# Kernel tuning notes

Measured on AMD Instinct MI355X. Metric: run time of the kernel, lower is better.

The kernel has to match this reference:

```python
import jax, jax.numpy as jnp
import numpy as np

DECAY = 0.99
EPS = 1e-5
BETA = 0.25

def _l2norm(v, axis=-1):
    # F.normalize: x / max(||x||, 1e-12)
    n = jnp.sqrt(jnp.sum(v * v, axis=axis, keepdims=True))
    return v / jnp.maximum(n, 1e-12)

def setup_inputs() -> dict:
    key = jax.random.key(0)
    k0, k1, k2, k3 = jax.random.split(key, 4)
    B, C, H, W, E, K = 8, 256, 64, 64, 32, 8192
    x = jax.random.normal(k0, (B, C, H, W), jnp.float32)
    Wq = jax.random.normal(k1, (E, C), jnp.float32) * 0.05  # 1x1 conv kernel
    bq = jnp.zeros((E,), jnp.float32)
    emb = jax.random.normal(k2, (K, E), jnp.float32)
    emb = _l2norm(emb, axis=1)  # matches F.normalize init in __init__
    ema_cluster_size = jnp.ones((K,), jnp.float32)
    ema_weight = emb  # consistent post-init EMA state
    return {"x": x, "Wq": Wq, "bq": bq, "embedding": emb,
            "ema_cluster_size": ema_cluster_size, "ema_weight": ema_weight}

def reference(x, Wq, bq, embedding, ema_cluster_size, ema_weight):
    B, C, H, W = x.shape
    E = Wq.shape[0]
    K = embedding.shape[0]
    # quant_conv: 1x1 conv == per-pixel linear
    z = jnp.einsum('bchw,ec->behw', x, Wq) + bq[None, :, None, None]  # [B,E,H,W]
    z_flat = z.transpose(0, 2, 3, 1).reshape(-1, E)  # [N,E]
    # get_idx(use_znorm=True): cosine similarity argmax (== argmin L2 on normalized)
    zn = _l2norm(z_flat, axis=1)
    en = _l2norm(embedding, axis=1)
    indices = jnp.argmax(zn @ en.T, axis=1)  # [N]
    # codebook gather (raw embedding, as in torch)
    z_q = embedding[indices].reshape(B, H, W, E).transpose(0, 3, 1, 2)  # [B,E,H,W]
    # EMA update (training path; scatter == one-hot.T @ z_flat / one-hot.sum)
    counts = jax.ops.segment_sum(jnp.ones((z_flat.shape[0],), z_flat.dtype), indices, num_segments=K)
    dw = jax.ops.segment_sum(z_flat, indices, num_segments=K)  # [K,E]
    new_cs = DECAY * ema_cluster_size + (1.0 - DECAY) * counts
    new_w = DECAY * ema_weight + (1.0 - DECAY) * dw
    n = jnp.sum(new_cs)
    cs_smoothed = (new_cs + EPS) / (n + K * EPS) * n
    new_embedding = new_w / cs_smoothed[:, None]
    # commitment loss + straight-through
    qloss = BETA * jnp.mean((jax.lax.stop_gradient(z_q) - z) ** 2)
    z_q_st = z + jax.lax.stop_gradient(z_q - z)
    return (z_q_st, indices.reshape(B, H, W), qloss, new_embedding, new_cs, new_w)
```

## Files before the change

### kernel.cpp

```cpp
#include <hip/hip_runtime.h>

#define B_ 8
#define C_ 256
#define HW_ 4096
#define E_ 32
#define K_ 8192
#define N_ 32768
#define NCHUNK 4
#define KC_ (K_ / NCHUNK)
#define NSTAGE (KC_ / 128)
#define KSEG 32
#define PIX 128

#define DECAY_ 0.99f
#define OMD_   0.01f
#define EPS_   1e-5f
#define BETA_  0.25f

#define O_ZQ   0
#define O_IDX  1048576
#define O_QL   1081344
#define O_NEMB 1081345
#define O_NCS  1343489
#define O_NW   1351681

#define WS_EH   0u
#define WS_EM   131072u
#define WS_Z    262144u
#define WS_PACK 1310720u
#define WS_PCS  1572864u
#define WS_QP   1572992u

typedef float f32x4 __attribute__((ext_vector_type(4)));
typedef short s16x8 __attribute__((ext_vector_type(8)));
typedef unsigned long long u64;

__device__ __forceinline__ unsigned short f2bf(float f) {
    unsigned u = __float_as_uint(f);
    u = u + 0x7fffu + ((u >> 16) & 1u);
    return (unsigned short)(u >> 16);
}
__device__ __forceinline__ float bf2f(unsigned short h) {
    return __uint_as_float(((unsigned)h) << 16);
}
__device__ __forceinline__ unsigned ford(float f) {
    unsigned u = __float_as_uint(f);
    return (u & 0x80000000u) ? ~u : (u | 0x80000000u);
}
__device__ __forceinline__ int imax(int a, int b) { return a > b ? a : b; }
__device__ __forceinline__ int imin(int a, int b) { return a < b ? a : b; }

__device__ __forceinline__ void gload_lds16(const void* g, void* l) {
    __builtin_amdgcn_global_load_lds(
        (const __attribute__((address_space(1))) unsigned int*)g,
        (__attribute__((address_space(3))) unsigned int*)l, 16, 0, 0);
}

__global__ __launch_bounds__(256) void k_pre(const float* __restrict__ emb,
                                             const float* __restrict__ cs,
                                             uint4* __restrict__ eh16,
                                             uint4* __restrict__ em16,
                                             float* __restrict__ part_cs,
                                             const float* __restrict__ x,
                                             const float* __restrict__ Wq,
                                             const float* __restrict__ bq,
                                             float* __restrict__ zout) {
    __shared__ float wqt[C_ * E_];
    int tid = threadIdx.x;

    if (blockIdx.x < 128) {
        int t4 = blockIdx.x * 256 + tid;
        int k = t4 >> 2, q = t4 & 3;
        const float4* r = (const float4*)(emb + (size_t)k * E_ + q * 8);
        float4 u0 = r[0], u1 = r[1];
        float ss = u0.x*u0.x + u0.y*u0.y + u0.z*u0.z + u0.w*u0.w
                 + u1.x*u1.x + u1.y*u1.y + u1.z*u1.z + u1.w*u1.w;
        ss += __shfl_xor(ss, 1, 64);
        ss += __shfl_xor(ss, 2, 64);
        float inv = 1.0f / fmaxf(sqrtf(ss), 1e-12f);

        float v[8] = {u0.x, u0.y, u0.z, u0.w, u1.x, u1.y, u1.z, u1.w};
        unsigned short h1a[8], h2a[8];
#pragma unroll
        for (int e = 0; e < 8; e++) {
            float en = v[e] * inv;
            unsigned short h1 = f2bf(en);
            float r1 = en - bf2f(h1);
            h1a[e] = h1; h2a[e] = f2bf(r1);
        }
        int t = k >> 4, c15 = k & 15;
        eh16[t * 64 + q * 16 + c15] = ((uint4*)h1a)[0];
        em16[t * 64 + q * 16 + c15] = ((uint4*)h2a)[0];

        if (tid < 64) {
            float cv = cs[blockIdx.x * 64 + tid];
#pragma unroll
            for (int off = 32; off > 0; off >>= 1) cv += __shfl_down(cv, off);
            if (tid == 0) part_cs[blockIdx.x] = cv;
        }
        return;
    }

    int zb = blockIdx.x - 128;
#pragma unroll
    for (int i = 0; i < 32; i++) {
        int g = i * 256 + tid;
        int e = g >> 8;
        int c = g & 255;
        wqt[c * E_ + e] = Wq[g];
    }
    __syncthreads();
    int lp = tid & 63, eg = tid >> 6;
    int n0 = zb * 128 + lp;
    int b  = n0 >> 12, hw = n0 & (HW_ - 1);
    const float* xp = x + (size_t)b * C_ * HW_ + hw;
    float a[16];
#pragma unroll
    for (int j = 0; j < 16; j++) a[j] = 0.f;
#pragma unroll 4
    for (int c = 0; c < C_; c++) {
        float xa = xp[(size_t)c * HW_];
        float xb = xp[(size_t)c * HW_ + 64];
        const float4* wr = (const float4*)(wqt + c * E_ + eg * 8);
        float4 w0 = wr[0], w1 = wr[1];
        a[0]  += xa * w0.x; a[1]  += xa * w0.y; a[2]  += xa * w0.z; a[3]  += xa * w0.w;
        a[4]  += xa * w1.x; a[5]  += xa * w1.y; a[6]  += xa * w1.z; a[7]  += xa * w1.w;
        a[8]  += xb * w0.x; a[9]  += xb * w0.y; a[10] += xb * w0.z; a[11] += xb * w0.w;
        a[12] += xb * w1.x; a[13] += xb * w1.y; a[14] += xb * w1.z; a[15] += xb * w1.w;
    }
    float bqv[8];
#pragma unroll
    for (int j = 0; j < 8; j++) bqv[j] = bq[eg * 8 + j];
    float4* zgA = (float4*)(zout + (size_t)n0 * E_ + eg * 8);
    float4* zgB = (float4*)(zout + (size_t)(n0 + 64) * E_ + eg * 8);
    zgA[0] = make_float4(a[0]+bqv[0],  a[1]+bqv[1],  a[2]+bqv[2],  a[3]+bqv[3]);
    zgA[1] = make_float4(a[4]+bqv[4],  a[5]+bqv[5],  a[6]+bqv[6],  a[7]+bqv[7]);
    zgB[0] = make_float4(a[8]+bqv[0],  a[9]+bqv[1],  a[10]+bqv[2], a[11]+bqv[3]);
    zgB[1] = make_float4(a[12]+bqv[4], a[13]+bqv[5], a[14]+bqv[6], a[15]+bqv[7]);
}

__global__ __launch_bounds__(512) void k_score_mfma(const float* __restrict__ zws,
                                                    const char* __restrict__ ehb,
                                                    const char* __restrict__ emb_b,
                                                    int2* __restrict__ pk2) {
    __shared__ __align__(16) char smem[32768];

    int tid  = threadIdx.x;
    int lane = tid & 63;
    int w    = tid >> 6;
    int chunk = blockIdx.y;

    s16x8 a1, a2;
    {
        int ploc = w * 16 + (lane & 15);
        int n0   = blockIdx.x * PIX + ploc;
        int e0   = (lane >> 4) * 8;
        const float4* zp = (const float4*)(zws + (size_t)n0 * E_ + e0);
        float4 z0 = zp[0], z1 = zp[1];
        float zz[8] = {z0.x, z0.y, z0.z, z0.w, z1.x, z1.y, z1.z, z1.w};
#pragma unroll
        for (int j = 0; j < 8; j++) {
            float zv = zz[j] * 134217728.0f;
            unsigned short h1 = f2bf(zv);
            float r1 = zv - bf2f(h1);
            a1[j] = (short)h1; a2[j] = (short)f2bf(r1);
        }
    }

    const char* srcp[2];
#pragma unroll
    for (int i = 0; i < 2; i++) {
        int d = i * 512 + tid;
        int pl = d >> 9, dd = d & 511;
        srcp[i] = (pl ? emb_b : ehb) + (size_t)chunk * (KC_ * 64) + dd * 16;
    }

#pragma unroll
    for (int i = 0; i < 2; i++)
        gload_lds16(srcp[i], smem + (i * 512 + tid) * 16);
    __syncthreads();

    int rbase = 8191 - chunk * KC_ - (lane & 15);
    int bq1[4], bq2[4];
#pragma unroll
    for (int j = 0; j < 4; j++) { bq1[j] = (int)0x80000000; bq2[j] = (int)0x80000000; }
    f32x4 zero4 = {0.f, 0.f, 0.f, 0.f};

    for (int st = 0; st < NSTAGE; st++) {
        if (st + 1 < NSTAGE) {
            char* dst = smem + ((st + 1) & 1) * 16384;
#pragma unroll
            for (int i = 0; i < 2; i++)
                gload_lds16(srcp[i] + (size_t)(st + 1) * 8192, dst + (i * 512 + tid) * 16);
        }
        const char* cur = smem + (st & 1) * 16384;
        int rst = rbase - st * 128;

#pragma unroll
        for (int g = 0; g < 2; g++) {
            int ct = g * 4;
            s16x8 b1[4], b2[4];
#pragma unroll
            for (int q = 0; q < 4; q++) {
                b1[q] = ((const s16x8*)(cur +        (ct + q) * 1024))[lane];
                b2[q] = ((const s16x8*)(cur + 8192 + (ct + q) * 1024))[lane];
            }
            f32x4 acc[4];
#pragma unroll
            for (int q = 0; q < 4; q++)
                acc[q] = __builtin_amdgcn_mfma_f32_16x16x32_bf16(a1, b1[q], zero4, 0, 0, 0);
#pragma unroll
            for (int q = 0; q < 4; q++)
                acc[q] = __builtin_amdgcn_mfma_f32_16x16x32_bf16(a1, b2[q], acc[q], 0, 0, 0);
#pragma unroll
            for (int q = 0; q < 4; q++)
                acc[q] = __builtin_amdgcn_mfma_f32_16x16x32_bf16(a2, b1[q], acc[q], 0, 0, 0);
            int r0 = rst - ct * 16;
#pragma unroll
            for (int j = 0; j < 4; j++) {
                int v0 = ((int)acc[0][j] & (int)0xFFFFE000) | r0;
                int v1 = ((int)acc[1][j] & (int)0xFFFFE000) | (r0 - 16);
                int v2 = ((int)acc[2][j] & (int)0xFFFFE000) | (r0 - 32);
                int v3 = ((int)acc[3][j] & (int)0xFFFFE000) | (r0 - 48);
                int hi = imax(imax(v0, v1), imax(v2, v3));
                int m  = imin(bq1[j], hi);
                bq1[j] = imax(bq1[j], hi);
                bq2[j] = imax(bq2[j], m);
            }
        }
        __syncthreads();
    }

#pragma unroll
    for (int off = 1; off < 16; off <<= 1) {
#pragma unroll
        for (int j = 0; j < 4; j++) {
            int o1 = __shfl_xor(bq1[j], off, 64);
            int o2 = __shfl_xor(bq2[j], off, 64);
            int m  = imin(bq1[j], o1);
            bq1[j] = imax(bq1[j], o1);
            bq2[j] = imax(imax(bq2[j], o2), m);
        }
    }
    if ((lane & 15) == 0) {
        int rowbase = blockIdx.x * PIX + w * 16 + (lane >> 4) * 4;
#pragma unroll
        for (int j = 0; j < 4; j++)
            pk2[(size_t)chunk * N_ + rowbase + j] = make_int2(bq1[j], bq2[j]);
    }
}

__device__ __forceinline__ float rescore(const float* __restrict__ emb, int k,
                                         const float* zrow) {
    const float4* r = (const float4*)(emb + (size_t)k * E_);
    float4 v[8];
    float ss = 0.f;
#pragma unroll
    for (int i = 0; i < 8; i++) {
        v[i] = r[i];
        ss += v[i].x * v[i].x + v[i].y * v[i].y + v[i].z * v[i].z + v[i].w * v[i].w;
    }
    float inv = 1.0f / fmaxf(sqrtf(ss), 1e-12f);
    const float4* zp = (const float4*)zrow;
    float sx = 0.f, sy = 0.f, sz = 0.f, sw = 0.f;
#pragma unroll
    for (int i = 0; i < 8; i++) {
        float4 e4 = make_float4(v[i].x * inv, v[i].y * inv, v[i].z * inv, v[i].w * inv);
        float4 zr = zp[i];
        sx += zr.x * e4.x; sy += zr.y * e4.y;
        sz += zr.z * e4.z; sw += zr.w * e4.w;
    }
    return (sx + sy) + (sz + sw);
}

__global__ __launch_bounds__(256) void k_scatter(const float* __restrict__ zws,
                                                 const int2* __restrict__ pk2,
                                                 const float* __restrict__ emb,
                                                 float* __restrict__ out_zq,
                                                 float* __restrict__ out_idx,
                                                 float* __restrict__ qpart) {
    __shared__ float zbuf[64 * E_];
    __shared__ int   idxs_s[64];
    __shared__ float red[4];
    int tid = threadIdx.x;

    const float4* zsrc = (const float4*)(zws + (size_t)blockIdx.x * 64 * E_);
    float4* zdst = (float4*)zbuf;
    zdst[tid]       = zsrc[tid];
    zdst[tid + 256] = zsrc[tid + 256];
    __syncthreads();

    {
        int p = tid >> 2, c4 = tid & 3;
        int nn = blockIdx.x * 64 + p;
        int2 c2 = pk2[(size_t)c4 * N_ + nn];
        u64 pkd = 0;
#pragma unroll
        for (int t = 0; t < 2; t++) {
            int raw = t ? c2.y : c2.x;
            int k = 8191 - (raw & 0x1fff);
            k = k < 0 ? 0 : (k > K_ - 1 ? K_ - 1 : k);
            float s = rescore(emb, k, zbuf + p * E_);
            u64 pk = ((u64)ford(s) << 32) | (unsigned)(K_ - 1 - k);
            pkd = pkd > pk ? pkd : pk;
        }
        u64 o = __shfl_xor(pkd, 1, 64); pkd = pkd > o ? pkd : o;
        o = __shfl_xor(pkd, 2, 64);     pkd = pkd > o ? pkd : o;
        if (c4 == 0) {
            int bi = K_ - 1 - (int)(unsigned)(pkd & 0xffffffffu);
            idxs_s[p] = bi;
            out_idx[nn] = (float)bi;
        }
    }
    __syncthreads();

    int lp = tid & 63, eg = tid >> 6;
    int n  = blockIdx.x * 64 + lp;
    int b  = n >> 12, hw = n & (HW_ - 1);
    int idx = idxs_s[lp];
    const float* er = emb + (size_t)idx * E_ + eg * 8;
    float* o = out_zq + (size_t)b * E_ * HW_ + (size_t)(eg * 8) * HW_ + hw;

    float sq = 0.f;
#pragma unroll
    for (int j = 0; j < 8; j++) {
        float zv = zbuf[lp * E_ + eg * 8 + j];
        float qf = er[j];
        float d = qf - zv;
        sq += d * d;
        o[(size_t)j * HW_] = qf;
    }

#pragma unroll
    for (int off = 32; off > 0; off >>= 1) sq += __shfl_down(sq, off);
    int lane = tid & 63, wid = tid >> 6;
    if (lane == 0) red[wid] = sq;
    __syncthreads();
    if (tid == 0) qpart[blockIdx.x] = red[0] + red[1] + red[2] + red[3];
}

__global__ __launch_bounds__(256) void k_dwfinal(const float* __restrict__ zws,
                                                 const float* __restrict__ idxf,
                                                 const float* __restrict__ cs,
                                                 const float* __restrict__ ew,
                                                 const float* __restrict__ part_cs,
                                                 const float* __restrict__ qpart,
                                                 float* __restrict__ out_nw,
                                                 float* __restrict__ out_nemb,
                                                 float* __restrict__ out_ncs,
                                                 float* __restrict__ out_ql) {
    __shared__ float acc[KSEG * E_];
    __shared__ int   cnt_s[KSEG];
    __shared__ int   plist[2048];
    __shared__ int   lcnt;
    __shared__ float nsum_s;
    int tid = threadIdx.x;
    int kbase = blockIdx.x * KSEG;

#pragma unroll
    for (int i = 0; i < KSEG * E_ / 256; i++) acc[tid + i * 256] = 0.f;
    if (tid < KSEG) cnt_s[tid] = 0;
    if (tid == 0) lcnt = 0;
    __syncthreads();

    const float4* idx4 = (const float4*)idxf;
    for (int tile = 0; tile < N_ / 2048; ++tile) {
        int pbase = tile * 2048 + tid * 8;
        float4 f0 = idx4[tile * 512 + tid * 2];
        float4 f1 = idx4[tile * 512 + tid * 2 + 1];
        float fs[8] = {f0.x, f0.y, f0.z, f0.w, f1.x, f1.y, f1.z, f1.w};
#pragma unroll
        for (int s = 0; s < 8; s++) {
            unsigned d = (unsigned)((int)fs[s] - kbase);
            if (d < (unsigned)KSEG) {
                int pos = atomicAdd(&lcnt, 1);
                plist[pos] = ((pbase + s) << 5) | (int)d;
                atomicAdd(cnt_s + (int)d, 1);
            }
        }
        __syncthreads();
        int cnt = lcnt;
        int e = tid & 31;
        for (int m = tid >> 5; m < cnt; m += 8) {
            int pk = plist[m];
            int nn = pk >> 5;
            float zv = zws[(size_t)nn * E_ + e];
            atomicAdd(acc + (pk & 31) * E_ + e, zv);
        }
        __syncthreads();
        if (tid == 0) lcnt = 0;
        __syncthreads();
    }

    if (tid < 64) {
        float s = part_cs[tid] + part_cs[tid + 64];
#pragma unroll
        for (int off = 32; off > 0; off >>= 1) s += __shfl_down(s, off);
        if (tid == 0) nsum_s = DECAY_ * s + OMD_ * (float)N_;
    }
    __syncthreads();
    float nsum = nsum_s;

#pragma unroll
    for (int i = 0; i < 4; i++) {
        int local = tid + i * 256;
        int kl = local >> 5, c = local & 31;
        int k = kbase + kl;
        float v = DECAY_ * ew[(size_t)k * E_ + c] + OMD_ * acc[local];
        out_nw[(size_t)k * E_ + c] = v;
        float csk = DECAY_ * cs[k] + OMD_ * (float)cnt_s[kl];
        float denom = (csk + EPS_) / (nsum + (float)K_ * EPS_) * nsum;
        out_nemb[(size_t)k * E_ + c] = v / denom;
        if (c == 0) out_ncs[k] = csk;
    }

    if (blockIdx.x == 0 && tid < 64) {
        float s = 0.f;
#pragma unroll
        for (int i = 0; i < 8; i++) s += qpart[tid + i * 64];
#pragma unroll
        for (int off = 32; off > 0; off >>= 1) s += __shfl_down(s, off);
        if (tid == 0) out_ql[0] = BETA_ * s / (float)(B_ * E_ * HW_);
    }
}

extern "C" void kernel_launch(void* const* d_in, const int* in_sizes, int n_in,
                              void* d_out, int out_size, void* d_ws, size_t ws_size,
                              hipStream_t stream) {
    const float* x   = (const float*)d_in[0];
    const float* Wq  = (const float*)d_in[1];
    const float* bq  = (const float*)d_in[2];
    const float* emb = (const float*)d_in[3];
    const float* cs  = (const float*)d_in[4];
    const float* ew  = (const float*)d_in[5];
    float* out = (float*)d_out;
    float* ws  = (float*)d_ws;

    k_pre<<<128 + N_ / 128, 256, 0, stream>>>(emb, cs,
        (uint4*)(ws + WS_EH), (uint4*)(ws + WS_EM), ws + WS_PCS,
        x, Wq, bq, ws + WS_Z);
    k_score_mfma<<<dim3(N_ / PIX, NCHUNK), 512, 0, stream>>>(ws + WS_Z,
        (const char*)(ws + WS_EH), (const char*)(ws + WS_EM),
        (int2*)(ws + WS_PACK));
    k_scatter<<<N_ / 64, 256, 0, stream>>>(ws + WS_Z,
        (const int2*)(ws + WS_PACK), emb,
        out + O_ZQ, out + O_IDX, ws + WS_QP);
    k_dwfinal<<<K_ / KSEG, 256, 0, stream>>>(ws + WS_Z, out + O_IDX, cs, ew,
                                             ws + WS_PCS, ws + WS_QP,
                                             out + O_NW, out + O_NEMB,
                                             out + O_NCS, out + O_QL);
}
```

Measured before the change: 197.5 us.

## Rebalance thread work in pre-pass and scatter kernels for higher parallelism

The prep kernel now runs 512-thread blocks: each thread normalizes a whole codebook row, and the z projection computes 4 output channels per thread instead of 8, doubling threads per pixel tile. The scatter kernel handles 32 pixels per block with one candidate rescore per thread, doubling the grid, and uses a wider shuffle reduction. Reduction sizes for the cluster-size partial sums (16 blocks) and the loss partials (1024 blocks) are adjusted to match. The aim is more parallelism and fewer serial dependencies, at the cost of more register pressure per thread in the codebook prep and more blocks to schedule.

Measured after the change: 198.0 us. No clear change (+0.3%).

```diff
diff --git a/kernel.cpp b/kernel.cpp
--- a/kernel.cpp
+++ b/kernel.cpp
@@ -56,7 +56,7 @@
         (__attribute__((address_space(3))) unsigned int*)l, 16, 0, 0);
 }
 
-__global__ __launch_bounds__(256) void k_pre(const float* __restrict__ emb,
+__global__ __launch_bounds__(512) void k_pre(const float* __restrict__ emb,
                                              const float* __restrict__ cs,
                                              uint4* __restrict__ eh16,
                                              uint4* __restrict__ em16,
@@ -66,45 +66,55 @@
                                              const float* __restrict__ bq,
                                              float* __restrict__ zout) {
     __shared__ float wqt[C_ * E_];
+    __shared__ float red8[8];
     int tid = threadIdx.x;
 
-    if (blockIdx.x < 128) {
-        int t4 = blockIdx.x * 256 + tid;
-        int k = t4 >> 2, q = t4 & 3;
-        const float4* r = (const float4*)(emb + (size_t)k * E_ + q * 8);
-        float4 u0 = r[0], u1 = r[1];
-        float ss = u0.x*u0.x + u0.y*u0.y + u0.z*u0.z + u0.w*u0.w
-                 + u1.x*u1.x + u1.y*u1.y + u1.z*u1.z + u1.w*u1.w;
-        ss += __shfl_xor(ss, 1, 64);
-        ss += __shfl_xor(ss, 2, 64);
+    if (blockIdx.x < 16) {
+        int k = blockIdx.x * 512 + tid;
+        const float4* r = (const float4*)(emb + (size_t)k * E_);
+        float v[E_];
+        float ss = 0.f;
+#pragma unroll
+        for (int i = 0; i < 8; i++) {
+            float4 t = r[i];
+            v[i*4+0] = t.x; v[i*4+1] = t.y; v[i*4+2] = t.z; v[i*4+3] = t.w;
+            ss += t.x*t.x + t.y*t.y + t.z*t.z + t.w*t.w;
+        }
         float inv = 1.0f / fmaxf(sqrtf(ss), 1e-12f);
-
-        float v[8] = {u0.x, u0.y, u0.z, u0.w, u1.x, u1.y, u1.z, u1.w};
-        unsigned short h1a[8], h2a[8];
-#pragma unroll
-        for (int e = 0; e < 8; e++) {
+        unsigned short h1a[E_], h2a[E_];
+#pragma unroll
+        for (int e = 0; e < E_; e++) {
             float en = v[e] * inv;
             unsigned short h1 = f2bf(en);
             float r1 = en - bf2f(h1);
             h1a[e] = h1; h2a[e] = f2bf(r1);
         }
         int t = k >> 4, c15 = k & 15;
-        eh16[t * 64 + q * 16 + c15] = ((uint4*)h1a)[0];
-        em16[t * 64 + q * 16 + c15] = ((uint4*)h2a)[0];
-
-        if (tid < 64) {
-            float cv = cs[blockIdx.x * 64 + tid];
-#pragma unroll
-            for (int off = 32; off > 0; off >>= 1) cv += __shfl_down(cv, off);
-            if (tid == 0) part_cs[blockIdx.x] = cv;
+#pragma unroll
+        for (int i = 0; i < 4; i++) {
+            eh16[t * 64 + i * 16 + c15] = ((uint4*)h1a)[i];
+            em16[t * 64 + i * 16 + c15] = ((uint4*)h2a)[i];
+        }
+
+        float cv = cs[blockIdx.x * 512 + tid];
+#pragma unroll
+        for (int off = 32; off > 0; off >>= 1) cv += __shfl_down(cv, off);
+        int lane = tid & 63, wid = tid >> 6;
+        if (lane == 0) red8[wid] = cv;
+        __syncthreads();
+        if (tid == 0) {
+            float s = 0.f;
+#pragma unroll
+            for (int i = 0; i < 8; i++) s += red8[i];
+            part_cs[blockIdx.x] = s;
         }
         return;
     }
 
-    int zb = blockIdx.x - 128;
-#pragma unroll
-    for (int i = 0; i < 32; i++) {
-        int g = i * 256 + tid;
+    int zb = blockIdx.x - 16;
+#pragma unroll
+    for (int i = 0; i < 16; i++) {
+        int g = i * 512 + tid;
         int e = g >> 8;
         int c = g & 255;
         wqt[c * E_ + e] = Wq[g];
@@ -114,29 +124,22 @@
     int n0 = zb * 128 + lp;
     int b  = n0 >> 12, hw = n0 & (HW_ - 1);
     const float* xp = x + (size_t)b * C_ * HW_ + hw;
-    float a[16];
-#pragma unroll
-    for (int j = 0; j < 16; j++) a[j] = 0.f;
+    float a[8];
+#pragma unroll
+    for (int j = 0; j < 8; j++) a[j] = 0.f;
 #pragma unroll 4
     for (int c = 0; c < C_; c++) {
         float xa = xp[(size_t)c * HW_];
         float xb = xp[(size_t)c * HW_ + 64];
-        const float4* wr = (const float4*)(wqt + c * E_ + eg * 8);
-        float4 w0 = wr[0], w1 = wr[1];
-        a[0]  += xa * w0.x; a[1]  += xa * w0.y; a[2]  += xa * w0.z; a[3]  += xa * w0.w;
-        a[4]  += xa * w1.x; a[5]  += xa * w1.y; a[6]  += xa * w1.z; a[7]  += xa * w1.w;
-        a[8]  += xb * w0.x; a[9]  += xb * w0.y; a[10] += xb * w0.z; a[11] += xb * w0.w;
-        a[12] += xb * w1.x; a[13] += xb * w1.y; a[14] += xb * w1.z; a[15] += xb * w1.w;
-    }
-    float bqv[8];
-#pragma unroll
-    for (int j = 0; j < 8; j++) bqv[j] = bq[eg * 8 + j];
-    float4* zgA = (float4*)(zout + (size_t)n0 * E_ + eg * 8);
-    float4* zgB = (float4*)(zout + (size_t)(n0 + 64) * E_ + eg * 8);
-    zgA[0] = make_float4(a[0]+bqv[0],  a[1]+bqv[1],  a[2]+bqv[2],  a[3]+bqv[3]);
-    zgA[1] = make_float4(a[4]+bqv[4],  a[5]+bqv[5],  a[6]+bqv[6],  a[7]+bqv[7]);
-    zgB[0] = make_float4(a[8]+bqv[0],  a[9]+bqv[1],  a[10]+bqv[2], a[11]+bqv[3]);
-    zgB[1] = make_float4(a[12]+bqv[4], a[13]+bqv[5], a[14]+bqv[6], a[15]+bqv[7]);
+        float4 wv = *(const float4*)(wqt + c * E_ + eg * 4);
+        a[0] += xa * wv.x; a[1] += xa * wv.y; a[2] += xa * wv.z; a[3] += xa * wv.w;
+        a[4] += xb * wv.x; a[5] += xb * wv.y; a[6] += xb * wv.z; a[7] += xb * wv.w;
+    }
+    float bq0 = bq[eg*4+0], bq1v = bq[eg*4+1], bq2v = bq[eg*4+2], bq3 = bq[eg*4+3];
+    *(float4*)(zout + (size_t)n0 * E_ + eg * 4) =
+        make_float4(a[0]+bq0, a[1]+bq1v, a[2]+bq2v, a[3]+bq3);
+    *(float4*)(zout + (size_t)(n0 + 64) * E_ + eg * 4) =
+        make_float4(a[4]+bq0, a[5]+bq1v, a[6]+bq2v, a[7]+bq3);
 }
 
 __global__ __launch_bounds__(512) void k_score_mfma(const float* __restrict__ zws,
@@ -279,34 +282,29 @@
                                                  float* __restrict__ out_zq,
                                                  float* __restrict__ out_idx,
                                                  float* __restrict__ qpart) {
-    __shared__ float zbuf[64 * E_];
-    __shared__ int   idxs_s[64];
+    __shared__ float zbuf[32 * E_];
+    __shared__ int   idxs_s[32];
     __shared__ float red[4];
     int tid = threadIdx.x;
 
-    const float4* zsrc = (const float4*)(zws + (size_t)blockIdx.x * 64 * E_);
-    float4* zdst = (float4*)zbuf;
-    zdst[tid]       = zsrc[tid];
-    zdst[tid + 256] = zsrc[tid + 256];
+    const float4* zsrc = (const float4*)(zws + (size_t)blockIdx.x * 32 * E_);
+    ((float4*)zbuf)[tid] = zsrc[tid];
     __syncthreads();
 
     {
-        int p = tid >> 2, c4 = tid & 3;
-        int nn = blockIdx.x * 64 + p;
-        int2 c2 = pk2[(size_t)c4 * N_ + nn];
-        u64 pkd = 0;
-#pragma unroll
-        for (int t = 0; t < 2; t++) {
-            int raw = t ? c2.y : c2.x;
-            int k = 8191 - (raw & 0x1fff);
-            k = k < 0 ? 0 : (k > K_ - 1 ? K_ - 1 : k);
-            float s = rescore(emb, k, zbuf + p * E_);
-            u64 pk = ((u64)ford(s) << 32) | (unsigned)(K_ - 1 - k);
-            pkd = pkd > pk ? pkd : pk;
-        }
+        int p = tid >> 3, c8 = tid & 7;
+        int chunk = c8 >> 1, top = c8 & 1;
+        int nn = blockIdx.x * 32 + p;
+        int2 c2 = pk2[(size_t)chunk * N_ + nn];
+        int raw = top ? c2.y : c2.x;
+        int k = 8191 - (raw & 0x1fff);
+        k = k < 0 ? 0 : (k > K_ - 1 ? K_ - 1 : k);
+        float s = rescore(emb, k, zbuf + p * E_);
+        u64 pkd = ((u64)ford(s) << 32) | (unsigned)(K_ - 1 - k);
         u64 o = __shfl_xor(pkd, 1, 64); pkd = pkd > o ? pkd : o;
         o = __shfl_xor(pkd, 2, 64);     pkd = pkd > o ? pkd : o;
-        if (c4 == 0) {
+        o = __shfl_xor(pkd, 4, 64);     pkd = pkd > o ? pkd : o;
+        if (c8 == 0) {
             int bi = K_ - 1 - (int)(unsigned)(pkd & 0xffffffffu);
             idxs_s[p] = bi;
             out_idx[nn] = (float)bi;
@@ -314,22 +312,23 @@
     }
     __syncthreads();
 
-    int lp = tid & 63, eg = tid >> 6;
-    int n  = blockIdx.x * 64 + lp;
+    int lp = tid & 31, eg = tid >> 5;
+    int n  = blockIdx.x * 32 + lp;
     int b  = n >> 12, hw = n & (HW_ - 1);
     int idx = idxs_s[lp];
-    const float* er = emb + (size_t)idx * E_ + eg * 8;
-    float* o = out_zq + (size_t)b * E_ * HW_ + (size_t)(eg * 8) * HW_ + hw;
-
-    float sq = 0.f;
-#pragma unroll
-    for (int j = 0; j < 8; j++) {
-        float zv = zbuf[lp * E_ + eg * 8 + j];
-        float qf = er[j];
-        float d = qf - zv;
-        sq += d * d;
-        o[(size_t)j * HW_] = qf;
-    }
+    float4 e4 = *(const float4*)(emb + (size_t)idx * E_ + eg * 4);
+    float* o = out_zq + (size_t)b * E_ * HW_ + (size_t)(eg * 4) * HW_ + hw;
+
+    float z0 = zbuf[lp * E_ + eg * 4 + 0];
+    float z1 = zbuf[lp * E_ + eg * 4 + 1];
+    float z2 = zbuf[lp * E_ + eg * 4 + 2];
+    float z3 = zbuf[lp * E_ + eg * 4 + 3];
+    o[0]                 = e4.x;
+    o[(size_t)1 * HW_]   = e4.y;
+    o[(size_t)2 * HW_]   = e4.z;
+    o[(size_t)3 * HW_]   = e4.w;
+    float d0 = e4.x - z0, d1 = e4.y - z1, d2 = e4.z - z2, d3 = e4.w - z3;
+    float sq = d0*d0 + d1*d1 + d2*d2 + d3*d3;
 
 #pragma unroll
     for (int off = 32; off > 0; off >>= 1) sq += __shfl_down(sq, off);
@@ -393,9 +392,11 @@
     }
 
     if (tid < 64) {
-        float s = part_cs[tid] + part_cs[tid + 64];
-#pragma unroll
-        for (int off = 32; off > 0; off >>= 1) s += __shfl_down(s, off);
+        float s = (tid < 16) ? part_cs[tid] : 0.f;
+        s += __shfl_down(s, 8);
+        s += __shfl_down(s, 4);
+        s += __shfl_down(s, 2);
+        s += __shfl_down(s, 1);
         if (tid == 0) nsum_s = DECAY_ * s + OMD_ * (float)N_;
     }
     __syncthreads();
@@ -417,7 +418,7 @@
     if (blockIdx.x == 0 && tid < 64) {
         float s = 0.f;
 #pragma unroll
-        for (int i = 0; i < 8; i++) s += qpart[tid + i * 64];
+        for (int i = 0; i < 16; i++) s += qpart[tid + i * 64];
 #pragma unroll
         for (int off = 32; off > 0; off >>= 1) s += __shfl_down(s, off);
         if (tid == 0) out_ql[0] = BETA_ * s / (float)(B_ * E_ * HW_);
@@ -436,13 +437,13 @@
     float* out = (float*)d_out;
     float* ws  = (float*)d_ws;
 
-    k_pre<<<128 + N_ / 128, 256, 0, stream>>>(emb, cs,
+    k_pre<<<16 + N_ / 128, 512, 0, stream>>>(emb, cs,
         (uint4*)(ws + WS_EH), (uint4*)(ws + WS_EM), ws + WS_PCS,
         x, Wq, bq, ws + WS_Z);
     k_score_mfma<<<dim3(N_ / PIX, NCHUNK), 512, 0, stream>>>(ws + WS_Z,
         (const char*)(ws + WS_EH), (const char*)(ws + WS_EM),
         (int2*)(ws + WS_PACK));
-    k_scatter<<<N_ / 64, 256, 0, stream>>>(ws + WS_Z,
+    k_scatter<<<N_ / 32, 256, 0, stream>>>(ws + WS_Z,
         (const int2*)(ws + WS_PACK), emb,
         out + O_ZQ, out + O_IDX, ws + WS_QP);
     k_dwfinal<<<K_ / KSEG, 256, 0, stream>>>(ws + WS_Z, out + O_IDX, cs, ew,
```
